# Performance work log

Hardware: AMD Instinct MI355X
Metric: run time of the kernel (lower is better)

Reference implementation:

```python
import jax, jax.numpy as jnp
import numpy as np

N_NODES = 50000
N_EDGES = 1200000
N_REL = 45
IN_C, HID_C, OUT_C = 64, 32, 16


def setup_inputs() -> dict:
    key = jax.random.key(0)
    ks = jax.random.split(key, 9)
    x = jax.random.normal(ks[0], (N_NODES, IN_C), dtype=jnp.float32)
    edge_index = jax.random.randint(ks[1], (2, N_EDGES), 0, N_NODES, dtype=jnp.int64)
    edge_type = jax.random.randint(ks[2], (N_EDGES,), 0, N_REL, dtype=jnp.int64)
    s = 0.05
    W1 = jax.random.normal(ks[3], (N_REL, IN_C, HID_C), dtype=jnp.float32) * s
    root1 = jax.random.normal(ks[4], (IN_C, HID_C), dtype=jnp.float32) * s
    b1 = jax.random.normal(ks[5], (HID_C,), dtype=jnp.float32) * s
    W2 = jax.random.normal(ks[6], (N_REL, HID_C, OUT_C), dtype=jnp.float32) * s
    root2 = jax.random.normal(ks[7], (HID_C, OUT_C), dtype=jnp.float32) * s
    b2 = jax.random.normal(ks[8], (OUT_C,), dtype=jnp.float32) * s
    return {"x": x, "edge_index": edge_index, "edge_type": edge_type,
            "W1": W1, "root1": root1, "b1": b1,
            "W2": W2, "root2": root2, "b2": b2}


def rgcn_conv(x, edge_index, edge_type, W, root, b):
    # PyG RGCNConv: out_i = x_i @ root + b + sum_r mean_{j in N_r(i)} (x_j @ W_r)
    N = x.shape[0]
    R = W.shape[0]
    src, dst = edge_index[0], edge_index[1]
    # per-relation transform of all nodes: [R, N, out]
    h = jnp.einsum('ni,rio->rno', x, W)
    # per-edge message: gather transformed src feature for edge's relation
    msg = h[edge_type, src]                      # [E, out]
    # segment id combines (relation, dst) for per-relation mean aggregation
    seg = edge_type * N + dst                    # [E]
    sums = jax.ops.segment_sum(msg, seg, num_segments=R * N)        # [R*N, out]
    cnt = jax.ops.segment_sum(jnp.ones((msg.shape[0],), x.dtype), seg,
                              num_segments=R * N)                   # [R*N]
    mean = sums / jnp.maximum(cnt, 1.0)[:, None]
    agg = mean.reshape(R, N, -1).sum(axis=0)     # sum over relations -> [N, out]
    return agg + x @ root + b


def reference(x, edge_index, edge_type, W1, root1, b1, W2, root2, b2):
    h = rgcn_conv(x, edge_index, edge_type, W1, root1, b1)
    h = jax.nn.relu(h)
    out = rgcn_conv(h, edge_index, edge_type, W2, root2, b2)
    return out
```

## Files before the change

kernel.cpp:

```cpp
#include <hip/hip_runtime.h>
#include <hip/hip_fp16.h>
#include <cstdint>
#include <cstddef>

#define NN   50000
#define NE   1200000
#define NR   45
#define INC  64
#define HIDC 32
#define OUTC 16
#define MAXE 1202880
#define NCHUNK (MAXE/64)
#define EPB 4096
#define NB  ((NE + EPB - 1) / EPB)
#define SEG 16
#define BPS ((NB + SEG - 1) / SEG)
#define QDW 3125
#define QDD 6250
#define NTILE ((NN + 255) / 256)
#define MS1 34
#define MS2 18

typedef _Float16 f16x8 __attribute__((ext_vector_type(8)));
typedef float    f32x4 __attribute__((ext_vector_type(4)));

union F16Bits { unsigned short u; _Float16 f; };
union ABFrag   { uint4 u; f16x8 f; };

__global__ __launch_bounds__(256) void preph_k(const float* __restrict__ W1,
                                               const float* __restrict__ W2,
                                               const float* __restrict__ x,
                                               const int* __restrict__ ei,
                                               const int* __restrict__ et,
                                               __half* __restrict__ W1f,
                                               __half* __restrict__ W2f,
                                               __half* __restrict__ xh,
                                               unsigned* __restrict__ ghist,
                                               unsigned* __restrict__ rsorted,
                                               unsigned* __restrict__ flagbuf) {
    __shared__ unsigned lh[NR];
    int t = threadIdx.x, b = blockIdx.x;
    if (t < NR) lh[t] = 0;
    __syncthreads();
    if (b < NB) {
        #pragma unroll
        for (int it = 0; it < EPB / 256; ++it) {
            int e = b * EPB + it * 256 + t;
            if (e < NE) {
                int r = et[e], src = ei[e], dst = ei[NE + e];
                if ((unsigned)r < NR && (unsigned)src < NN && (unsigned)dst < NN)
                    atomicAdd(&lh[r], 1u);
            }
        }
    }
    __syncthreads();
    if (b < NB && t < NR) ghist[b * NR + t] = lh[t];
    int g = b * 256 + t;
    int gthreads = gridDim.x * 256;
    for (int i = g; i < MAXE; i += gthreads) rsorted[i] = 0xFFFFFFFFu;
    if (b == 0) flagbuf[t] = 0;
    if (g < NR * 2048) {
        int r = g >> 11, rem = g & 2047;
        int kb = rem >> 10, nb = (rem >> 9) & 1;
        int lane = (rem >> 3) & 63, j = rem & 7;
        int k = kb * 32 + (lane >> 4) * 8 + j;
        int n = nb * 16 + (lane & 15);
        W1f[g] = __float2half(W1[(r * INC + k) * HIDC + n]);
    }
    if (g < NR * 512) {
        int r = g >> 9, rem = g & 511;
        int lane = (rem >> 3) & 63, j = rem & 7;
        int k = (lane >> 4) * 8 + j;
        int n = lane & 15;
        W2f[g] = __float2half(W2[(r * HIDC + k) * OUTC + n]);
    }
    if (g < NN * INC / 2) {
        float2 f = ((const float2*)x)[g];
        union { __half2 h; unsigned u; } cv;
        cv.h = __floats2half2_rn(f.x, f.y);
        ((unsigned*)xh)[g] = cv.u;
    }
}

__global__ __launch_bounds__(1024) void rss_k(const int* __restrict__ ei,
                                              const int* __restrict__ et,
                                              unsigned* __restrict__ ghist,
                                              unsigned* __restrict__ rbase,
                                              unsigned* __restrict__ rngs,
                                              int* __restrict__ chunkrel,
                                              unsigned* __restrict__ rsorted,
                                              unsigned* __restrict__ flagbuf) {
    __shared__ unsigned part[NR * SEG];
    __shared__ unsigned relbase[NR + 1];
    __shared__ unsigned reltot[NR];
    __shared__ unsigned lbase[NR], lcur[NR];
    int t = threadIdx.x, bx = blockIdx.x;
    if (bx == 0) {
        int r = t / SEG, sg = t % SEG;
        if (t < NR * SEG) {
            unsigned s = 0;
            int b0 = sg * BPS, b1 = b0 + BPS; if (b1 > NB) b1 = NB;
            for (int b = b0; b < b1; ++b) s += ghist[b * NR + r];
            part[t] = s;
        }
        __syncthreads();
        if (t < NR) {
            unsigned run = 0;
            #pragma unroll
            for (int s = 0; s < SEG; ++s) {
                unsigned v = part[t * SEG + s];
                part[t * SEG + s] = run;
                run += v;
            }
            reltot[t] = run;
        }
        __syncthreads();
        if (t == 0) {
            unsigned acc = 0;
            for (int rr = 0; rr < NR; ++rr) {
                relbase[rr] = acc;
                acc += ((reltot[rr] + 63u) >> 6) << 6;
            }
            relbase[NR] = acc;
        }
        __syncthreads();
        if (t < NR * SEG) {
            unsigned run = part[t] + relbase[r];
            int b0 = sg * BPS, b1 = b0 + BPS; if (b1 > NB) b1 = NB;
            for (int b = b0; b < b1; ++b) {
                unsigned v = ghist[b * NR + r];
                ghist[b * NR + r] = run;
                run += v;
            }
        }
        __syncthreads();
        for (int i = t; i < NR * NB; i += 1024) {
            int rr = i / NB, b = i % NB;
            atomicExch(&rbase[i], ghist[b * NR + rr]);
        }
        if (t < NR) {
            rngs[2 * t]     = relbase[t];
            rngs[2 * t + 1] = relbase[t] + reltot[t];
        }
        for (int c = t; c < NCHUNK; c += 1024) {
            unsigned pos = (unsigned)c << 6;
            int lo = 0, hi = NR - 1;
            while (lo < hi) {
                int mid = (lo + hi + 1) >> 1;
                if (relbase[mid] <= pos) lo = mid; else hi = mid - 1;
            }
            chunkrel[c] = lo;
        }
        __syncthreads();
        __threadfence();
        if (t == 0) atomicExch(&flagbuf[0], 1u);
    }
    if (bx != 0 && t == 0) {
        while (atomicAdd(&flagbuf[0], 0u) == 0u) { }
    }
    __syncthreads();
    if (t < NR) { lbase[t] = atomicAdd(&rbase[t * NB + bx], 0u); lcur[t] = 0; }
    __syncthreads();
    #pragma unroll
    for (int it = 0; it < EPB / 1024; ++it) {
        int e = bx * EPB + it * 1024 + t;
        if (e < NE) {
            int r = et[e], src = ei[e], dst = ei[NE + e];
            if ((unsigned)r < NR && (unsigned)src < NN && (unsigned)dst < NN) {
                unsigned local = atomicAdd(&lcur[r], 1u);
                rsorted[lbase[r] + local] = (unsigned)src | ((unsigned)dst << 16);
            }
        }
    }
}

__global__ __launch_bounds__(1024) void relcnt_k(const unsigned* __restrict__ rsorted,
                                                 const unsigned* __restrict__ rngs,
                                                 unsigned short* __restrict__ cnt16,
                                                 unsigned short* __restrict__ rank16) {
    __shared__ unsigned lds[QDW];
    int r = blockIdx.x >> 3, q = blockIdx.x & 7, t = threadIdx.x;
    unsigned base = rngs[2 * r], end = rngs[2 * r + 1];
    unsigned dlo = q * QDD, dhi = dlo + QDD;
    for (int w = t; w < QDW; w += 1024) lds[w] = 0;
    __syncthreads();
    for (unsigned s = base + t; s < end; s += 1024) {
        unsigned d = rsorted[s] >> 16;
        if (d >= dlo && d < dhi) {
            unsigned off = d - dlo;
            atomicAdd(&lds[off >> 1], (off & 1) ? 0x10000u : 1u);
        }
    }
    __syncthreads();
    unsigned* __restrict__ cp = (unsigned*)(cnt16 + (size_t)r * NN + dlo);
    for (int w = t; w < QDW; w += 1024) cp[w] = lds[w];
    __syncthreads();
    for (int w = t; w < QDW; w += 1024) lds[w] = 0;
    __syncthreads();
    for (unsigned s = base + t; s < end; s += 1024) {
        unsigned d = rsorted[s] >> 16;
        if (d >= dlo && d < dhi) {
            unsigned off = d - dlo;
            unsigned old = atomicAdd(&lds[off >> 1], (off & 1) ? 0x10000u : 1u);
            rank16[s] = (unsigned short)((off & 1) ? (old >> 16) : (old & 0xFFFFu));
        }
    }
}

__global__ __launch_bounds__(256) void dp_k(const unsigned short* __restrict__ cnt16,
                                            unsigned* __restrict__ packed,
                                            unsigned* __restrict__ rowptr,
                                            unsigned* __restrict__ flags) {
    __shared__ unsigned wsum[4];
    __shared__ unsigned excl_s;
    int t = threadIdx.x, b = blockIdx.x;
    int lane = t & 63, wv = t >> 6;
    int dst = b * 256 + t;
    unsigned deg = 0;
    if (dst < NN) {
        unsigned run = 0;
        #pragma unroll 5
        for (int r = 0; r < NR; ++r) {
            unsigned c = cnt16[(size_t)r * NN + dst];
            F16Bits fb; fb.f = (_Float16)(c ? 1.0f / (float)c : 0.0f);
            packed[(size_t)r * NN + dst] = (run & 0xFFFFu) | ((unsigned)fb.u << 16);
            run += c;
        }
        deg = run;
    }
    unsigned s = deg;
    #pragma unroll
    for (int off = 1; off < 64; off <<= 1) {
        unsigned n = __shfl_up(s, off);
        if (lane >= off) s += n;
    }
    if (lane == 63) wsum[wv] = s;
    __syncthreads();
    unsigned waveoff = 0;
    if (wv > 0) waveoff += wsum[0];
    if (wv > 1) waveoff += wsum[1];
    if (wv > 2) waveoff += wsum[2];
    unsigned blockT = wsum[0] + wsum[1] + wsum[2] + wsum[3];
    unsigned local_excl = waveoff + s - deg;
    if (t == 0) {
        if (b == 0) {
            excl_s = 0;
            atomicExch(&flags[0], 0x80000000u | blockT);
        } else {
            atomicExch(&flags[b], 0x40000000u | blockT);
            unsigned ex = 0;
            int p = b - 1;
            while (p >= 0) {
                unsigned f = atomicAdd(&flags[p], 0u);
                unsigned st = f >> 30;
                if (st == 0) continue;
                ex += f & 0x3FFFFFFFu;
                if (st >= 2) break;
                --p;
            }
            excl_s = ex;
            atomicExch(&flags[b], 0x80000000u | (ex + blockT));
        }
    }
    __syncthreads();
    unsigned ex = excl_s;
    if (dst < NN) rowptr[dst] = ex + local_excl;
    if (b == (int)gridDim.x - 1 && t == 0) rowptr[NN] = ex + blockT;
}

__global__ __launch_bounds__(256) void finalize_k(const unsigned* __restrict__ rsorted,
                                                  const unsigned short* __restrict__ rank16,
                                                  const unsigned* __restrict__ packed,
                                                  const unsigned* __restrict__ rowptr,
                                                  const int* __restrict__ chunkrel,
                                                  uint2* __restrict__ pedges) {
    int s = blockIdx.x * 256 + threadIdx.x;
    if (s >= MAXE) return;
    unsigned v = rsorted[s];
    unsigned dst = v >> 16;
    if (dst >= NN) { pedges[s] = make_uint2(0u, 0x80000000u); return; }
    int r = chunkrel[s >> 6];
    unsigned pk = packed[(size_t)r * NN + dst];
    unsigned dpos = rowptr[dst] + (pk & 0xFFFFu) + (unsigned)rank16[s];
    pedges[s] = make_uint2((v & 0xFFFFu) | (pk & 0xFFFF0000u),
                           dpos | ((unsigned)r << 25));
}

__global__ __launch_bounds__(256) void msg1_k(const __half* __restrict__ xh,
                                              const __half* __restrict__ W1f,
                                              const uint2* __restrict__ pedges,
                                              __half* __restrict__ msg) {
    __shared__ float lmsg[4 * 16 * MS1];
    int tid = threadIdx.x;
    int wv = tid >> 6, lane = tid & 63;
    int wave = (blockIdx.x * 256 + tid) >> 6;
    if (wave >= NCHUNK) return;
    int e = (wave << 6) + lane;
    uint2 er = pedges[e];
    int w1 = (int)er.y;
    int rel = __builtin_amdgcn_readfirstlane((w1 >> 25) & 63);
    F16Bits fb; fb.u = (unsigned short)(er.x >> 16);
    float sc = (float)fb.f;
    int src = er.x & 0xFFFF;
    int drow = (w1 < 0) ? NE : (w1 & 0x1FFFFFF);
    const uint4* __restrict__ wf = (const uint4*)W1f + (size_t)rel * 256;
    ABFrag b00, b01, b10, b11;
    b00.u = wf[0 * 64 + lane];
    b01.u = wf[1 * 64 + lane];
    b10.u = wf[2 * 64 + lane];
    b11.u = wf[3 * 64 + lane];
    int quad = lane >> 4, col = lane & 15;
    float* __restrict__ lwave = lmsg + wv * (16 * MS1);
    #pragma unroll
    for (int tl = 0; tl < 4; ++tl) {
        int s = __shfl(src, tl * 16 + col);
        const uint4* __restrict__ xp = (const uint4*)(xh + (size_t)s * INC) + quad;
        ABFrag a0, a1;
        a0.u = xp[0];
        a1.u = xp[4];
        f32x4 acc0 = {0.f, 0.f, 0.f, 0.f}, acc1 = {0.f, 0.f, 0.f, 0.f};
        acc0 = __builtin_amdgcn_mfma_f32_16x16x32_f16(a0.f, b00.f, acc0, 0, 0, 0);
        acc0 = __builtin_amdgcn_mfma_f32_16x16x32_f16(a1.f, b10.f, acc0, 0, 0, 0);
        acc1 = __builtin_amdgcn_mfma_f32_16x16x32_f16(a0.f, b01.f, acc1, 0, 0, 0);
        acc1 = __builtin_amdgcn_mfma_f32_16x16x32_f16(a1.f, b11.f, acc1, 0, 0, 0);
        float* __restrict__ lt = lwave + (quad * 4) * MS1;
        #pragma unroll
        for (int i = 0; i < 4; ++i) {
            lt[i * MS1 + col]      = acc0[i];
            lt[i * MS1 + col + 16] = acc1[i];
        }
        if ((lane >> 4) == tl) {
            const float* __restrict__ myrow = lwave + (lane & 15) * MS1;
            unsigned um[16];
            #pragma unroll
            for (int k = 0; k < 16; ++k) {
                float2 vv = *(const float2*)(myrow + 2 * k);
                union { __half2 h; unsigned u; } cv;
                cv.h = __floats2half2_rn(vv.x * sc, vv.y * sc);
                um[k] = cv.u;
            }
            uint4* __restrict__ mrow = (uint4*)(msg + (size_t)drow * HIDC);
            #pragma unroll
            for (int q = 0; q < 4; ++q)
                mrow[q] = make_uint4(um[4*q], um[4*q+1], um[4*q+2], um[4*q+3]);
        }
    }
}

__global__ __launch_bounds__(256) void msg2_k(const __half* __restrict__ hh,
                                              const __half* __restrict__ W2f,
                                              const uint2* __restrict__ pedges,
                                              __half* __restrict__ msg) {
    __shared__ float lmsg[4 * 16 * MS2];
    int tid = threadIdx.x;
    int wv = tid >> 6, lane = tid & 63;
    int wave = (blockIdx.x * 256 + tid) >> 6;
    if (wave >= NCHUNK) return;
    int e = (wave << 6) + lane;
    uint2 er = pedges[e];
    int w1 = (int)er.y;
    int rel = __builtin_amdgcn_readfirstlane((w1 >> 25) & 63);
    F16Bits fb; fb.u = (unsigned short)(er.x >> 16);
    float sc = (float)fb.f;
    int src = er.x & 0xFFFF;
    int drow = (w1 < 0) ? NE : (w1 & 0x1FFFFFF);
    ABFrag bf;
    bf.u = ((const uint4*)W2f + (size_t)rel * 64)[lane];
    int quad = lane >> 4, col = lane & 15;
    float* __restrict__ lwave = lmsg + wv * (16 * MS2);
    #pragma unroll
    for (int tl = 0; tl < 4; ++tl) {
        int s = __shfl(src, tl * 16 + col);
        ABFrag a;
        a.u = *((const uint4*)(hh + (size_t)s * HIDC) + quad);
        f32x4 acc = {0.f, 0.f, 0.f, 0.f};
        acc = __builtin_amdgcn_mfma_f32_16x16x32_f16(a.f, bf.f, acc, 0, 0, 0);
        float* __restrict__ lt = lwave + (quad * 4) * MS2;
        #pragma unroll
        for (int i = 0; i < 4; ++i) lt[i * MS2 + col] = acc[i];
        if ((lane >> 4) == tl) {
            const float* __restrict__ myrow = lwave + (lane & 15) * MS2;
            unsigned um[8];
            #pragma unroll
            for (int k = 0; k < 8; ++k) {
                float2 vv = *(const float2*)(myrow + 2 * k);
                union { __half2 h; unsigned u; } cv;
                cv.h = __floats2half2_rn(vv.x * sc, vv.y * sc);
                um[k] = cv.u;
            }
            uint4* __restrict__ mrow = (uint4*)(msg + (size_t)drow * OUTC);
            mrow[0] = make_uint4(um[0], um[1], um[2], um[3]);
            mrow[1] = make_uint4(um[4], um[5], um[6], um[7]);
        }
    }
}

__global__ __launch_bounds__(256) void gather1_k(const float* __restrict__ x,
                                                 const float* __restrict__ root1,
                                                 const float* __restrict__ b1,
                                                 const __half* __restrict__ msg,
                                                 const unsigned* __restrict__ rowptr,
                                                 __half* __restrict__ hh) {
    __shared__ float sr[INC * HIDC];
    for (int k = threadIdx.x; k < INC * HIDC; k += 256) sr[k] = root1[k];
    __syncthreads();
    int wid = (blockIdx.x * 256 + threadIdx.x) >> 6;
    int lane = threadIdx.x & 63;
    int c2 = lane & 15, sub = lane >> 4;
    unsigned k0 = rowptr[wid], k1 = rowptr[wid + 1];
    float accx = 0.f, accy = 0.f;
    for (unsigned k = k0 + sub; k < k1; k += 4) {
        union { __half2 hh2; unsigned u; } cv;
        cv.u = ((const unsigned*)(msg + (size_t)k * HIDC))[c2];
        float2 f = __half22float2(cv.hh2);
        accx += f.x; accy += f.y;
    }
    const float4* __restrict__ xp = (const float4*)(x + (size_t)wid * INC + sub * 16);
    #pragma unroll
    for (int q = 0; q < 4; ++q) {
        float4 xr = xp[q];
        const float* xs = (const float*)&xr;
        #pragma unroll
        for (int j = 0; j < 4; ++j) {
            int in = sub * 16 + q * 4 + j;
            float2 rt = *(const float2*)&sr[in * HIDC + 2 * c2];
            accx = fmaf(xs[j], rt.x, accx);
            accy = fmaf(xs[j], rt.y, accy);
        }
    }
    accx += __shfl_xor(accx, 16); accy += __shfl_xor(accy, 16);
    accx += __shfl_xor(accx, 32); accy += __shfl_xor(accy, 32);
    if (sub == 0) {
        float2 bb = *(const float2*)&b1[2 * c2];
        float vx = accx + bb.x, vy = accy + bb.y;
        union { __half2 h2; unsigned u; } cv;
        cv.h2 = __floats2half2_rn(vx > 0.f ? vx : 0.f, vy > 0.f ? vy : 0.f);
        ((unsigned*)hh)[(size_t)wid * (HIDC / 2) + c2] = cv.u;
    }
}

__global__ __launch_bounds__(256) void gather2_k(const __half* __restrict__ hh,
                                                 const float* __restrict__ root2,
                                                 const float* __restrict__ b2,
                                                 const __half* __restrict__ msg,
                                                 const unsigned* __restrict__ rowptr,
                                                 float* __restrict__ out) {
    __shared__ float sr[HIDC * OUTC];
    for (int k = threadIdx.x; k < HIDC * OUTC; k += 256) sr[k] = root2[k];
    __syncthreads();
    int wid = (blockIdx.x * 256 + threadIdx.x) >> 6;
    int lane = threadIdx.x & 63;
    int c2 = lane & 7, sub = lane >> 3;
    unsigned k0 = rowptr[wid], k1 = rowptr[wid + 1];
    float accx = 0.f, accy = 0.f;
    for (unsigned k = k0 + sub; k < k1; k += 8) {
        union { __half2 hh2; unsigned u; } cv;
        cv.u = ((const unsigned*)(msg + (size_t)k * OUTC))[c2];
        float2 f = __half22float2(cv.hh2);
        accx += f.x; accy += f.y;
    }
    uint2 hw = *(const uint2*)(hh + (size_t)wid * HIDC + sub * 4);
    union { __half2 h2; unsigned u; } ca, cb;
    ca.u = hw.x; cb.u = hw.y;
    float2 ha = __half22float2(ca.h2), hb = __half22float2(cb.h2);
    float hs[4] = { ha.x, ha.y, hb.x, hb.y };
    #pragma unroll
    for (int j = 0; j < 4; ++j) {
        int in = sub * 4 + j;
        float2 rt = *(const float2*)&sr[in * OUTC + 2 * c2];
        accx = fmaf(hs[j], rt.x, accx);
        accy = fmaf(hs[j], rt.y, accy);
    }
    accx += __shfl_xor(accx, 8);  accy += __shfl_xor(accy, 8);
    accx += __shfl_xor(accx, 16); accy += __shfl_xor(accy, 16);
    accx += __shfl_xor(accx, 32); accy += __shfl_xor(accy, 32);
    if (sub == 0) {
        float2 bb = *(const float2*)&b2[2 * c2];
        *(float2*)&out[(size_t)wid * OUTC + 2 * c2] =
            make_float2(accx + bb.x, accy + bb.y);
    }
}

extern "C" void kernel_launch(void* const* d_in, const int* in_sizes, int n_in,
                              void* d_out, int out_size, void* d_ws, size_t ws_size,
                              hipStream_t stream) {
    const float* x     = (const float*)d_in[0];
    const int*   ei    = (const int*)d_in[1];
    const int*   et    = (const int*)d_in[2];
    const float* W1    = (const float*)d_in[3];
    const float* root1 = (const float*)d_in[4];
    const float* b1    = (const float*)d_in[5];
    const float* W2    = (const float*)d_in[6];
    const float* root2 = (const float*)d_in[7];
    const float* b2    = (const float*)d_in[8];
    float* out = (float*)d_out;

    char* ws = (char*)d_ws;
    size_t o = 0;
    auto alloc = [&](size_t bytes) -> char* {
        char* p = ws + o;
        o = (o + bytes + 255) & ~(size_t)255;
        return p;
    };
    unsigned* rsorted = (unsigned*)alloc((size_t)MAXE * 4);
    unsigned* flagbuf = (unsigned*)alloc(256 * 4);
    unsigned* ghist   = (unsigned*)alloc((size_t)NR * NB * 4);
    unsigned* rbase   = (unsigned*)alloc((size_t)NR * NB * 4);
    unsigned* rngs    = (unsigned*)alloc((size_t)NR * 2 * 4);
    int*      chunkrel= (int*)     alloc((size_t)NCHUNK * 4);
    unsigned short* rank16 = (unsigned short*)alloc((size_t)MAXE * 2);
    unsigned short* cnt16  = (unsigned short*)alloc((size_t)NR * NN * 2);
    unsigned* packed  = (unsigned*)alloc((size_t)NR * NN * 4);
    unsigned* rowptr  = (unsigned*)alloc(((size_t)NN + 1) * 4);
    uint2*    pedges  = (uint2*)   alloc((size_t)MAXE * 8);
    __half*   W1f     = (__half*)  alloc((size_t)NR * 2048 * 2);
    __half*   W2f     = (__half*)  alloc((size_t)NR * 512 * 2);
    __half*   xh      = (__half*)  alloc((size_t)NN * INC * 2);
    __half*   hh      = (__half*)  alloc((size_t)NN * HIDC * 2);
    char*     msgraw  = alloc(((size_t)NE + 1) * 64);
    __half*   msg1    = (__half*)msgraw;
    __half*   msg2    = (__half*)msgraw;

    int prep_grid = NN * INC / 2 / 256;
    preph_k   <<<prep_grid, 256, 0, stream>>>(W1, W2, x, ei, et, W1f, W2f, xh,
                                              ghist, rsorted, flagbuf);
    rss_k     <<<NB, 1024, 0, stream>>>(ei, et, ghist, rbase, rngs, chunkrel,
                                        rsorted, flagbuf);
    relcnt_k  <<<8 * NR, 1024, 0, stream>>>(rsorted, rngs, cnt16, rank16);
    dp_k      <<<NTILE, 256, 0, stream>>>(cnt16, packed, rowptr, flagbuf + 32);
    finalize_k<<<(MAXE + 255) / 256, 256, 0, stream>>>(rsorted, rank16, packed,
                                                       rowptr, chunkrel, pedges);
    msg1_k    <<<(MAXE + 255) / 256, 256, 0, stream>>>(xh, W1f, pedges, msg1);
    gather1_k <<<NN * 64 / 256, 256, 0, stream>>>(x, root1, b1, msg1, rowptr, hh);
    msg2_k    <<<(MAXE + 255) / 256, 256, 0, stream>>>(hh, W2f, pedges, msg2);
    gather2_k <<<NN * 64 / 256, 256, 0, stream>>>(hh, root2, b2, msg2, rowptr, out);
}
```

Baseline: 336.7 us.

## Replace spin-flag scan with redundant per-block histogram prefix in scatter kernel

Removes the block-0 global prefix scan and the spin-wait flag that made every other block wait on it. Instead each block's 45 threads walk the whole per-block histogram (NB≈293 entries per relation) to compute both its own offset and the relation totals. The serial dependency on block 0 and the rbase buffer both go away. In exchange every block repeats roughly 13K global reads of ghist.

```diff
diff --git a/kernel.cpp b/kernel.cpp
--- a/kernel.cpp
+++ b/kernel.cpp
@@ -13,8 +13,6 @@
 #define NCHUNK (MAXE/64)
 #define EPB 4096
 #define NB  ((NE + EPB - 1) / EPB)
-#define SEG 16
-#define BPS ((NB + SEG - 1) / SEG)
 #define QDW 3125
 #define QDD 6250
 #define NTILE ((NN + 255) / 256)
@@ -82,84 +80,38 @@
     }
 }
 
-__global__ __launch_bounds__(1024) void rss_k(const int* __restrict__ ei,
-                                              const int* __restrict__ et,
-                                              unsigned* __restrict__ ghist,
-                                              unsigned* __restrict__ rbase,
-                                              unsigned* __restrict__ rngs,
-                                              int* __restrict__ chunkrel,
-                                              unsigned* __restrict__ rsorted,
-                                              unsigned* __restrict__ flagbuf) {
-    __shared__ unsigned part[NR * SEG];
+__global__ __launch_bounds__(1024) void scat_k(const int* __restrict__ ei,
+                                               const int* __restrict__ et,
+                                               const unsigned* __restrict__ ghist,
+                                               unsigned* __restrict__ rngs,
+                                               int* __restrict__ chunkrel,
+                                               unsigned* __restrict__ rsorted) {
+    __shared__ unsigned reltot[NR];
+    __shared__ unsigned mypart[NR];
     __shared__ unsigned relbase[NR + 1];
-    __shared__ unsigned reltot[NR];
     __shared__ unsigned lbase[NR], lcur[NR];
     int t = threadIdx.x, bx = blockIdx.x;
-    if (bx == 0) {
-        int r = t / SEG, sg = t % SEG;
-        if (t < NR * SEG) {
-            unsigned s = 0;
-            int b0 = sg * BPS, b1 = b0 + BPS; if (b1 > NB) b1 = NB;
-            for (int b = b0; b < b1; ++b) s += ghist[b * NR + r];
-            part[t] = s;
-        }
-        __syncthreads();
-        if (t < NR) {
-            unsigned run = 0;
-            #pragma unroll
-            for (int s = 0; s < SEG; ++s) {
-                unsigned v = part[t * SEG + s];
-                part[t * SEG + s] = run;
-                run += v;
-            }
-            reltot[t] = run;
-        }
-        __syncthreads();
-        if (t == 0) {
-            unsigned acc = 0;
-            for (int rr = 0; rr < NR; ++rr) {
-                relbase[rr] = acc;
-                acc += ((reltot[rr] + 63u) >> 6) << 6;
-            }
-            relbase[NR] = acc;
-        }
-        __syncthreads();
-        if (t < NR * SEG) {
-            unsigned run = part[t] + relbase[r];
-            int b0 = sg * BPS, b1 = b0 + BPS; if (b1 > NB) b1 = NB;
-            for (int b = b0; b < b1; ++b) {
-                unsigned v = ghist[b * NR + r];
-                ghist[b * NR + r] = run;
-                run += v;
-            }
-        }
-        __syncthreads();
-        for (int i = t; i < NR * NB; i += 1024) {
-            int rr = i / NB, b = i % NB;
-            atomicExch(&rbase[i], ghist[b * NR + rr]);
-        }
-        if (t < NR) {
-            rngs[2 * t]     = relbase[t];
-            rngs[2 * t + 1] = relbase[t] + reltot[t];
-        }
-        for (int c = t; c < NCHUNK; c += 1024) {
-            unsigned pos = (unsigned)c << 6;
-            int lo = 0, hi = NR - 1;
-            while (lo < hi) {
-                int mid = (lo + hi + 1) >> 1;
-                if (relbase[mid] <= pos) lo = mid; else hi = mid - 1;
-            }
-            chunkrel[c] = lo;
-        }
-        __syncthreads();
-        __threadfence();
-        if (t == 0) atomicExch(&flagbuf[0], 1u);
-    }
-    if (bx != 0 && t == 0) {
-        while (atomicAdd(&flagbuf[0], 0u) == 0u) { }
-    }
-    __syncthreads();
-    if (t < NR) { lbase[t] = atomicAdd(&rbase[t * NB + bx], 0u); lcur[t] = 0; }
+    if (t < NR) {
+        unsigned total = 0, part = 0;
+        for (int b = 0; b < NB; ++b) {
+            if (b == bx) part = total;
+            total += ghist[b * NR + t];
+        }
+        reltot[t] = total;
+        mypart[t] = part;
+        lcur[t] = 0;
+    }
+    __syncthreads();
+    if (t == 0) {
+        unsigned acc = 0;
+        for (int r = 0; r < NR; ++r) {
+            relbase[r] = acc;
+            acc += ((reltot[r] + 63u) >> 6) << 6;
+        }
+        relbase[NR] = acc;
+    }
+    __syncthreads();
+    if (t < NR) lbase[t] = relbase[t] + mypart[t];
     __syncthreads();
     #pragma unroll
     for (int it = 0; it < EPB / 1024; ++it) {
@@ -170,6 +122,21 @@
                 unsigned local = atomicAdd(&lcur[r], 1u);
                 rsorted[lbase[r] + local] = (unsigned)src | ((unsigned)dst << 16);
             }
+        }
+    }
+    if (bx == 0) {
+        if (t < NR) {
+            rngs[2 * t]     = relbase[t];
+            rngs[2 * t + 1] = relbase[t] + reltot[t];
+        }
+        for (int c = t; c < NCHUNK; c += 1024) {
+            unsigned pos = (unsigned)c << 6;
+            int lo = 0, hi = NR - 1;
+            while (lo < hi) {
+                int mid = (lo + hi + 1) >> 1;
+                if (relbase[mid] <= pos) lo = mid; else hi = mid - 1;
+            }
+            chunkrel[c] = lo;
         }
     }
 }
@@ -505,7 +472,6 @@
     unsigned* rsorted = (unsigned*)alloc((size_t)MAXE * 4);
     unsigned* flagbuf = (unsigned*)alloc(256 * 4);
     unsigned* ghist   = (unsigned*)alloc((size_t)NR * NB * 4);
-    unsigned* rbase   = (unsigned*)alloc((size_t)NR * NB * 4);
     unsigned* rngs    = (unsigned*)alloc((size_t)NR * 2 * 4);
     int*      chunkrel= (int*)     alloc((size_t)NCHUNK * 4);
     unsigned short* rank16 = (unsigned short*)alloc((size_t)MAXE * 2);
@@ -524,8 +490,7 @@
     int prep_grid = NN * INC / 2 / 256;
     preph_k   <<<prep_grid, 256, 0, stream>>>(W1, W2, x, ei, et, W1f, W2f, xh,
                                               ghist, rsorted, flagbuf);
-    rss_k     <<<NB, 1024, 0, stream>>>(ei, et, ghist, rbase, rngs, chunkrel,
-                                        rsorted, flagbuf);
+    scat_k    <<<NB, 1024, 0, stream>>>(ei, et, ghist, rngs, chunkrel, rsorted);
     relcnt_k  <<<8 * NR, 1024, 0, stream>>>(rsorted, rngs, cnt16, rank16);
     dp_k      <<<NTILE, 256, 0, stream>>>(cnt16, packed, rowptr, flagbuf + 32);
     finalize_k<<<(MAXE + 255) / 256, 256, 0, stream>>>(rsorted, rank16, packed,
```

Result: faster. 327.3 us (-2.8%).
